# Performance work log

Measured on AMD Instinct MI355X. Metric: run time of the kernel, lower is better.

## Reference

```python
import jax, jax.numpy as jnp
import numpy as np

N_NODES = 100000
N_EDGES = 1600000


def setup_inputs() -> dict:
    key = jax.random.key(0)
    ks = jax.random.split(key, 10)
    return {
        "src": jax.random.randint(ks[0], (N_EDGES,), 0, N_NODES, dtype=jnp.int32),
        "dst": jax.random.randint(ks[1], (N_EDGES,), 0, N_NODES, dtype=jnp.int32),
        "logits": jax.random.normal(ks[2], (N_NODES, 64), jnp.float32),
        "features": jax.random.normal(ks[3], (N_NODES, 512), jnp.float32),
        "proj_W": jax.random.normal(ks[4], (512, 128), jnp.float32) * 0.04,
        "proj_b": jnp.zeros((128,), jnp.float32),
        "deg_table": jax.random.normal(ks[5], (512, 64), jnp.float32) * 0.1,
        "W1": jax.random.normal(ks[6], (256, 128), jnp.float32) * 0.06,
        "b1": jnp.zeros((128,), jnp.float32),
        "W2": jax.random.normal(ks[7], (128, 64), jnp.float32) * 0.09,
        "b2": jnp.zeros((64,), jnp.float32),
    }


def _graph_conv(x, W, b, src, dst, out_deg, in_deg, n):
    # DGL GraphConv, norm='both': scale src by out_deg^-1/2, SpMM sum over
    # edges (src -> dst), scale dst by in_deg^-1/2, then bias. Weight is
    # applied before aggregation when in_feats > out_feats (true here).
    cs = jax.lax.rsqrt(jnp.maximum(out_deg, 1.0))  # [N]
    cd = jax.lax.rsqrt(jnp.maximum(in_deg, 1.0))   # [N]
    h = x * cs[:, None]
    if W.shape[0] > W.shape[1]:
        h = h @ W
        agg = jax.ops.segment_sum(h[src], dst, num_segments=n)
    else:
        agg = jax.ops.segment_sum(h[src], dst, num_segments=n) @ W
    return agg * cd[:, None] + b


def reference(src, dst, logits, features, proj_W, proj_b, deg_table, W1, b1, W2, b2):
    n = logits.shape[0]
    ones = jnp.ones(src.shape, jnp.float32)
    out_deg = jax.ops.segment_sum(ones, src, num_segments=n)  # [N]
    in_deg = jax.ops.segment_sum(ones, dst, num_segments=n)   # [N]

    feat = features @ proj_W + proj_b                          # [N, 128]
    deg_idx = (in_deg + out_deg).astype(jnp.int32)             # [N]
    deg_emb = deg_table[deg_idx]                               # [N, 64]
    x = jnp.concatenate([logits, feat, deg_emb], axis=-1)      # [N, 256]

    x = _graph_conv(x, W1, b1, src, dst, out_deg, in_deg, n)
    x = jax.nn.relu(x)  # dropout omitted (eval mode)
    x = _graph_conv(x, W2, b2, src, dst, out_deg, in_deg, n)
    return x
```

## Files before the change

### kernel.cpp

```cpp
#include <hip/hip_runtime.h>
#include <cstdint>
#include <cstddef>


typedef short short8 __attribute__((ext_vector_type(8)));
typedef float f32x4 __attribute__((ext_vector_type(4)));

__device__ __forceinline__ unsigned short f2bf(float f) {
    unsigned u = __float_as_uint(f);
    u += 0x7fff + ((u >> 16) & 1);
    return (unsigned short)(u >> 16);
}
__device__ __forceinline__ float bf2f(unsigned short s) {
    return __uint_as_float(((unsigned)s) << 16);
}

__device__ __forceinline__ void split_f4(float4 a, float4 b, short8& hv, short8& lv) {
    float f[8] = {a.x, a.y, a.z, a.w, b.x, b.y, b.z, b.w};
#pragma unroll
    for (int i = 0; i < 8; ++i) {
        unsigned u = __float_as_uint(f[i]);
        hv[i] = (short)(u >> 16);
        float r = f[i] - __uint_as_float(u & 0xffff0000u);
        lv[i] = (short)(__float_as_uint(r) >> 16);
    }
}


__global__ __launch_bounds__(256) void k_bcount(
    const int* __restrict__ src, const int* __restrict__ dst, int E,
    int* __restrict__ dcount, int* __restrict__ scount)
{
    __shared__ int dh[128], sh_[128];
    int t = threadIdx.x;
    if (t < 128) { dh[t] = 0; sh_[t] = 0; }
    __syncthreads();
    int e0 = blockIdx.x * 4096;
#pragma unroll
    for (int i = 0; i < 16; ++i) {
        int idx = e0 + t + i * 256;
        if (idx < E) {
            atomicAdd(&dh[dst[idx] >> 10], 1);
            atomicAdd(&sh_[src[idx] >> 10], 1);
        }
    }
    __syncthreads();
    if (t < 128) {
        if (dh[t]) atomicAdd(&dcount[t], dh[t]);
        if (sh_[t]) atomicAdd(&scount[t], sh_[t]);
    }
}

__global__ __launch_bounds__(128) void k_bscan(
    const int* __restrict__ dcount, const int* __restrict__ scount, int nb,
    int E, int* __restrict__ dboff, int* __restrict__ sboff,
    int* __restrict__ dcur, int* __restrict__ scur,
    int* __restrict__ rowp, int N)
{
    __shared__ int sh[128];
    int t = threadIdx.x;
    int v = (t < nb) ? dcount[t] : 0;
    sh[t] = v;
    __syncthreads();
    for (int off = 1; off < 128; off <<= 1) {
        int x = (t >= off) ? sh[t - off] : 0;
        __syncthreads();
        sh[t] += x;
        __syncthreads();
    }
    if (t < nb) { int e = sh[t] - v; dboff[t] = e; dcur[t] = e; }
    __syncthreads();
    int v2 = (t < nb) ? scount[t] : 0;
    sh[t] = v2;
    __syncthreads();
    for (int off = 1; off < 128; off <<= 1) {
        int x = (t >= off) ? sh[t - off] : 0;
        __syncthreads();
        sh[t] += x;
        __syncthreads();
    }
    if (t < nb) { int e = sh[t] - v2; sboff[t] = e; scur[t] = e; }
    if (t == 0) rowp[N] = E;
}

__global__ __launch_bounds__(256) void k_scatter2(
    const int* __restrict__ src, const int* __restrict__ dst, int E,
    int* __restrict__ dcur, int* __restrict__ scur,
    unsigned* __restrict__ ebuf, unsigned short* __restrict__ sbuf, int nb)
{
    __shared__ int dh[128], dbase[128], sh_[128], sbase[128];
    int t = threadIdx.x;
    int e0 = blockIdx.x * 4096;
    if (t < 128) { dh[t] = 0; sh_[t] = 0; }
    __syncthreads();
    int s_[16], d_[16];
#pragma unroll
    for (int i = 0; i < 16; ++i) {
        int idx = e0 + t + i * 256;
        if (idx < E) {
            s_[i] = src[idx];
            d_[i] = dst[idx];
            atomicAdd(&dh[d_[i] >> 10], 1);
            atomicAdd(&sh_[s_[i] >> 10], 1);
        } else d_[i] = -1;
    }
    __syncthreads();
    if (t < nb) {
        if (dh[t]) dbase[t] = atomicAdd(&dcur[t], dh[t]);
        if (sh_[t]) sbase[t] = atomicAdd(&scur[t], sh_[t]);
    }
    __syncthreads();
    if (t < 128) { dh[t] = 0; sh_[t] = 0; }
    __syncthreads();
#pragma unroll
    for (int i = 0; i < 16; ++i) {
        if (d_[i] >= 0) {
            int b = d_[i] >> 10;
            int p = dbase[b] + atomicAdd(&dh[b], 1);
            ebuf[p] = (unsigned)s_[i] | ((unsigned)(d_[i] & 1023) << 17);
            int bs = s_[i] >> 10;
            int q = sbase[bs] + atomicAdd(&sh_[bs], 1);
            sbuf[q] = (unsigned short)(s_[i] & 1023);
        }
    }
}

__global__ __launch_bounds__(512) void k_bucket_dst(
    const unsigned* __restrict__ ebuf, const int* __restrict__ dboff,
    const int* __restrict__ dcount, int* __restrict__ ind,
    int* __restrict__ rowp, int* __restrict__ csr, int N)
{
    __shared__ int cnt[1024];
    __shared__ int sums[512];
    int b = blockIdx.x;
    int nb0 = b << 10;
    int ncnt = min(1024, N - nb0);
    int t = threadIdx.x;
    cnt[t] = 0; cnt[t + 512] = 0;
    __syncthreads();
    int lo = dboff[b], hi = lo + dcount[b];
    for (int idx = lo + t; idx < hi; idx += 512)
        atomicAdd(&cnt[ebuf[idx] >> 17], 1);
    __syncthreads();
    int c0 = cnt[2 * t], c1 = cnt[2 * t + 1];
    sums[t] = c0 + c1;
    __syncthreads();
    for (int off = 1; off < 512; off <<= 1) {
        int x = (t >= off) ? sums[t - off] : 0;
        __syncthreads();
        sums[t] += x;
        __syncthreads();
    }
    int excl = sums[t] - (c0 + c1);
    int r0 = lo + excl, r1 = r0 + c0;
    if (2 * t < ncnt)     { rowp[nb0 + 2 * t] = r0;     ind[nb0 + 2 * t] = c0; }
    if (2 * t + 1 < ncnt) { rowp[nb0 + 2 * t + 1] = r1; ind[nb0 + 2 * t + 1] = c1; }
    __syncthreads();
    cnt[2 * t] = r0; cnt[2 * t + 1] = r1;
    __syncthreads();
    for (int idx = lo + t; idx < hi; idx += 512) {
        unsigned e = ebuf[idx];
        int p = atomicAdd(&cnt[e >> 17], 1);
        csr[p] = (int)(e & 0x1FFFF);
    }
}

__global__ __launch_bounds__(512) void k_bucket_src(
    const unsigned short* __restrict__ sbuf, const int* __restrict__ sboff,
    const int* __restrict__ scount, const int* __restrict__ ind,
    float* __restrict__ cs, float* __restrict__ cd, int* __restrict__ didx,
    int N)
{
    __shared__ int cnt[1024];
    int b = blockIdx.x;
    int nb0 = b << 10;
    int ncnt = min(1024, N - nb0);
    int t = threadIdx.x;
    cnt[t] = 0; cnt[t + 512] = 0;
    __syncthreads();
    int lo = sboff[b], hi = lo + scount[b];
    for (int idx = lo + t; idx < hi; idx += 512)
        atomicAdd(&cnt[sbuf[idx]], 1);
    __syncthreads();
#pragma unroll
    for (int k = 0; k < 2; ++k) {
        int loc = t + k * 512;
        if (loc < ncnt) {
            int od = cnt[loc];
            int id = ind[nb0 + loc];
            cs[nb0 + loc] = rsqrtf((float)(od > 0 ? od : 1));
            cd[nb0 + loc] = rsqrtf((float)(id > 0 ? id : 1));
            int d = od + id;
            didx[nb0 + loc] = d > 511 ? 511 : d;
        }
    }
}

__global__ __launch_bounds__(256) void k_wf(
    const float* __restrict__ projW, const float* __restrict__ projb,
    const float* __restrict__ W1, float* __restrict__ WF,
    float* __restrict__ cb)
{
    if (blockIdx.x == 256) {
        int j = threadIdx.x;
        if (j < 128) {
            float s = 0.f;
            for (int m = 0; m < 128; ++m)
                s = fmaf(projb[m], W1[(size_t)(64 + m) * 128 + j], s);
            cb[j] = s;
        }
        return;
    }
    int idx = blockIdx.x * 256 + threadIdx.x;
    int k = idx >> 7, j = idx & 127;
    const float* a = projW + (size_t)k * 128;
    float s = 0.f;
#pragma unroll 8
    for (int m = 0; m < 128; ++m) s = fmaf(a[m], W1[(size_t)(64 + m) * 128 + j], s);
    WF[idx] = s;
}

__global__ __launch_bounds__(256) void k_wt(
    const float* __restrict__ WF, const float* __restrict__ W1,
    const float* __restrict__ W2,
    unsigned short* __restrict__ wtf_hi, unsigned short* __restrict__ wtf_lo,
    unsigned short* __restrict__ w2tf_hi, unsigned short* __restrict__ w2tf_lo)
{
    int idx = blockIdx.x * 256 + threadIdx.x;
    if (idx < 81920) {
        int e = idx & 7;
        int lane = (idx >> 3) & 63;
        int ci = (idx >> 9) & 7;
        int t = idx >> 12;
        int j = ci * 16 + (lane & 15);
        int k = t * 32 + (lane >> 4) * 8 + e;
        float v;
        if (k < 512) v = WF[(size_t)k * 128 + j];
        else if (k < 576) v = W1[(size_t)(k - 512) * 128 + j];
        else v = W1[(size_t)(192 + (k - 576)) * 128 + j];
        unsigned short h = f2bf(v);
        wtf_hi[idx] = h;
        float r = v - bf2f(h);
        wtf_lo[idx] = (unsigned short)(__float_as_uint(r) >> 16);
    } else if (idx < 90112) {
        int i2 = idx - 81920;
        int e = i2 & 7;
        int lane = (i2 >> 3) & 63;
        int ci = (i2 >> 9) & 3;
        int t = i2 >> 11;
        int j = ci * 16 + (lane & 15);
        int k = t * 32 + (lane >> 4) * 8 + e;
        float v = W2[(size_t)k * 64 + j];
        unsigned short h = f2bf(v);
        w2tf_hi[i2] = h;
        float r = v - bf2f(h);
        w2tf_lo[i2] = (unsigned short)(__float_as_uint(r) >> 16);
    }
}

__global__ __launch_bounds__(256, 4) void k_h1(
    const float* __restrict__ logits, const float* __restrict__ features,
    const float* __restrict__ deg_table, const int* __restrict__ didx,
    const unsigned short* __restrict__ wtf_hi, const unsigned short* __restrict__ wtf_lo,
    const float* __restrict__ cb, const float* __restrict__ cs,
    unsigned short* __restrict__ h1, int N)
{
    constexpr int NT = 20;
    __shared__ __align__(16) short Bh[2][4096];
    __shared__ __align__(16) short Bl[2][4096];
    int tid = threadIdx.x;
    int lane = tid & 63, w = tid >> 6;
    int fr = lane & 15, kg = lane >> 4;
    int i0 = blockIdx.x * 64 + w * 16;
    int r0 = i0 + fr;  if (r0 >= N) r0 = N - 1;
    int dd0 = didx[r0];

    f32x4 acc[8];
#pragma unroll
    for (int ci = 0; ci < 8; ++ci) acc[ci] = (f32x4)0.f;

    auto aptr = [&](int t) -> const float* {
        if (t < 16) return features  + (size_t)r0 * 512 + t * 32 + kg * 8;
        if (t < 18) return logits    + (size_t)r0 * 64 + (t - 16) * 32 + kg * 8;
        return deg_table + (size_t)dd0 * 64 + (t - 18) * 32 + kg * 8;
    };

    float4 ac0, ac1, an0, an1;
    uint4 sbh0, sbh1, sbl0, sbl1;

    {
        const unsigned short* g = wtf_hi + tid * 8;
        sbh0 = *(const uint4*)g;
        sbh1 = *(const uint4*)(g + 2048);
        const unsigned short* g2 = wtf_lo + tid * 8;
        sbl0 = *(const uint4*)g2;
        sbl1 = *(const uint4*)(g2 + 2048);
        *(uint4*)&Bh[0][tid * 8] = sbh0;
        *(uint4*)&Bh[0][2048 + tid * 8] = sbh1;
        *(uint4*)&Bl[0][tid * 8] = sbl0;
        *(uint4*)&Bl[0][2048 + tid * 8] = sbl1;
        const float* p = aptr(0);
        ac0 = *(const float4*)p;  ac1 = *(const float4*)(p + 4);
    }
    __syncthreads();

    for (int t = 0; t < NT; ++t) {
        int cbuf = t & 1;
        if (t + 1 < NT) {
            const unsigned short* g = wtf_hi + (size_t)(t + 1) * 4096 + tid * 8;
            sbh0 = *(const uint4*)g;
            sbh1 = *(const uint4*)(g + 2048);
            const unsigned short* g2 = wtf_lo + (size_t)(t + 1) * 4096 + tid * 8;
            sbl0 = *(const uint4*)g2;
            sbl1 = *(const uint4*)(g2 + 2048);
            const float* p = aptr(t + 1);
            an0 = *(const float4*)p;  an1 = *(const float4*)(p + 4);
        }
        short8 ah, al;
        split_f4(ac0, ac1, ah, al);
#pragma unroll
        for (int ci = 0; ci < 8; ++ci) {
            short8 bh = *(const short8*)&Bh[cbuf][ci * 512 + lane * 8];
            short8 bl = *(const short8*)&Bl[cbuf][ci * 512 + lane * 8];
            acc[ci] = __builtin_amdgcn_mfma_f32_16x16x32_bf16(ah, bh, acc[ci], 0, 0, 0);
            acc[ci] = __builtin_amdgcn_mfma_f32_16x16x32_bf16(al, bh, acc[ci], 0, 0, 0);
            acc[ci] = __builtin_amdgcn_mfma_f32_16x16x32_bf16(ah, bl, acc[ci], 0, 0, 0);
        }
        if (t + 1 < NT) {
            *(uint4*)&Bh[cbuf ^ 1][tid * 8] = sbh0;
            *(uint4*)&Bh[cbuf ^ 1][2048 + tid * 8] = sbh1;
            *(uint4*)&Bl[cbuf ^ 1][tid * 8] = sbl0;
            *(uint4*)&Bl[cbuf ^ 1][2048 + tid * 8] = sbl1;
            ac0 = an0;  ac1 = an1;
        }
        __syncthreads();
    }

    float cbv[8];
#pragma unroll
    for (int ci = 0; ci < 8; ++ci) cbv[ci] = cb[ci * 16 + fr];
#pragma unroll
    for (int j = 0; j < 4; ++j) {
        int row = i0 + kg * 4 + j;
        if (row < N) {
            float scv = cs[row];
#pragma unroll
            for (int ci = 0; ci < 8; ++ci) {
                h1[(size_t)row * 128 + ci * 16 + fr] =
                    f2bf(scv * (acc[ci][j] + cbv[ci]));
            }
        }
    }
}

__global__ __launch_bounds__(256) void k_agg1(
    const unsigned short* __restrict__ h1, const int* __restrict__ rowp,
    const int* __restrict__ csr, const float* __restrict__ cd,
    const float* __restrict__ b1, float* __restrict__ y, int N)
{
    int i = blockIdx.x * 8 + (threadIdx.x >> 5);
    if (i >= N) return;
    int lane = threadIdx.x & 31;
    int s0 = rowp[i], s1 = rowp[i + 1];
    float a0 = 0.f, a1 = 0.f, a2 = 0.f, a3 = 0.f;
    int e = s0;
    for (; e + 8 <= s1; e += 8) {
        uint2 v0 = *(const uint2*)(h1 + (size_t)csr[e + 0] * 128 + lane * 4);
        uint2 v1 = *(const uint2*)(h1 + (size_t)csr[e + 1] * 128 + lane * 4);
        uint2 v2 = *(const uint2*)(h1 + (size_t)csr[e + 2] * 128 + lane * 4);
        uint2 v3 = *(const uint2*)(h1 + (size_t)csr[e + 3] * 128 + lane * 4);
        uint2 v4 = *(const uint2*)(h1 + (size_t)csr[e + 4] * 128 + lane * 4);
        uint2 v5 = *(const uint2*)(h1 + (size_t)csr[e + 5] * 128 + lane * 4);
        uint2 v6 = *(const uint2*)(h1 + (size_t)csr[e + 6] * 128 + lane * 4);
        uint2 v7 = *(const uint2*)(h1 + (size_t)csr[e + 7] * 128 + lane * 4);
        a0 += ((__uint_as_float(v0.x << 16) + __uint_as_float(v1.x << 16)) +
               (__uint_as_float(v2.x << 16) + __uint_as_float(v3.x << 16))) +
              ((__uint_as_float(v4.x << 16) + __uint_as_float(v5.x << 16)) +
               (__uint_as_float(v6.x << 16) + __uint_as_float(v7.x << 16)));
        a1 += ((__uint_as_float(v0.x & 0xffff0000u) + __uint_as_float(v1.x & 0xffff0000u)) +
               (__uint_as_float(v2.x & 0xffff0000u) + __uint_as_float(v3.x & 0xffff0000u))) +
              ((__uint_as_float(v4.x & 0xffff0000u) + __uint_as_float(v5.x & 0xffff0000u)) +
               (__uint_as_float(v6.x & 0xffff0000u) + __uint_as_float(v7.x & 0xffff0000u)));
        a2 += ((__uint_as_float(v0.y << 16) + __uint_as_float(v1.y << 16)) +
               (__uint_as_float(v2.y << 16) + __uint_as_float(v3.y << 16))) +
              ((__uint_as_float(v4.y << 16) + __uint_as_float(v5.y << 16)) +
               (__uint_as_float(v6.y << 16) + __uint_as_float(v7.y << 16)));
        a3 += ((__uint_as_float(v0.y & 0xffff0000u) + __uint_as_float(v1.y & 0xffff0000u)) +
               (__uint_as_float(v2.y & 0xffff0000u) + __uint_as_float(v3.y & 0xffff0000u))) +
              ((__uint_as_float(v4.y & 0xffff0000u) + __uint_as_float(v5.y & 0xffff0000u)) +
               (__uint_as_float(v6.y & 0xffff0000u) + __uint_as_float(v7.y & 0xffff0000u)));
    }
    for (; e < s1; ++e) {
        uint2 v = *(const uint2*)(h1 + (size_t)csr[e] * 128 + lane * 4);
        a0 += __uint_as_float(v.x << 16);
        a1 += __uint_as_float(v.x & 0xffff0000u);
        a2 += __uint_as_float(v.y << 16);
        a3 += __uint_as_float(v.y & 0xffff0000u);
    }
    float cdi = cd[i];
    float4 bv = *(const float4*)(b1 + lane * 4);
    float4 o;
    o.x = fmaxf(fmaf(a0, cdi, bv.x), 0.f);
    o.y = fmaxf(fmaf(a1, cdi, bv.y), 0.f);
    o.z = fmaxf(fmaf(a2, cdi, bv.z), 0.f);
    o.w = fmaxf(fmaf(a3, cdi, bv.w), 0.f);
    *(float4*)(y + (size_t)i * 128 + lane * 4) = o;
}

__global__ __launch_bounds__(256, 3) void k_h2(
    const float* __restrict__ y,
    const unsigned short* __restrict__ w2tf_hi, const unsigned short* __restrict__ w2tf_lo,
    const float* __restrict__ cs, unsigned short* __restrict__ h2, int N)
{
    constexpr int NT = 4;
    __shared__ __align__(16) short B2h[8192];
    __shared__ __align__(16) short B2l[8192];
    int tid = threadIdx.x;
    int lane = tid & 63, w = tid >> 6;
    int fr = lane & 15, kg = lane >> 4;
    int i0 = blockIdx.x * 128 + w * 32;
    int r0 = i0 + fr;       if (r0 >= N) r0 = N - 1;
    int r1 = i0 + 16 + fr;  if (r1 >= N) r1 = N - 1;
    const float* a0 = y + (size_t)r0 * 128 + kg * 8;
    const float* a1 = y + (size_t)r1 * 128 + kg * 8;

#pragma unroll
    for (int i = 0; i < 4; ++i) {
        *(uint4*)&B2h[(i * 256 + tid) * 8] = *(const uint4*)(w2tf_hi + (size_t)(i * 256 + tid) * 8);
        *(uint4*)&B2l[(i * 256 + tid) * 8] = *(const uint4*)(w2tf_lo + (size_t)(i * 256 + tid) * 8);
    }
    __syncthreads();

    f32x4 acc[2][4];
#pragma unroll
    for (int ri = 0; ri < 2; ++ri)
#pragma unroll
        for (int ci = 0; ci < 4; ++ci) acc[ri][ci] = (f32x4)0.f;

    float4 ar00 = *(const float4*)(a0);
    float4 ar01 = *(const float4*)(a0 + 4);
    float4 ar10 = *(const float4*)(a1);
    float4 ar11 = *(const float4*)(a1 + 4);

    for (int t = 0; t < NT; ++t) {
        short8 ah0, al0, ah1, al1;
        split_f4(ar00, ar01, ah0, al0);
        split_f4(ar10, ar11, ah1, al1);
        if (t + 1 < NT) {
            ar00 = *(const float4*)(a0 + (t + 1) * 32);
            ar01 = *(const float4*)(a0 + (t + 1) * 32 + 4);
            ar10 = *(const float4*)(a1 + (t + 1) * 32);
            ar11 = *(const float4*)(a1 + (t + 1) * 32 + 4);
        }
#pragma unroll
        for (int ci = 0; ci < 4; ++ci) {
            short8 bh = *(const short8*)&B2h[((t * 4 + ci) * 64 + lane) * 8];
            short8 bl = *(const short8*)&B2l[((t * 4 + ci) * 64 + lane) * 8];
            acc[0][ci] = __builtin_amdgcn_mfma_f32_16x16x32_bf16(ah0, bh, acc[0][ci], 0, 0, 0);
            acc[0][ci] = __builtin_amdgcn_mfma_f32_16x16x32_bf16(al0, bh, acc[0][ci], 0, 0, 0);
            acc[0][ci] = __builtin_amdgcn_mfma_f32_16x16x32_bf16(ah0, bl, acc[0][ci], 0, 0, 0);
            acc[1][ci] = __builtin_amdgcn_mfma_f32_16x16x32_bf16(ah1, bh, acc[1][ci], 0, 0, 0);
            acc[1][ci] = __builtin_amdgcn_mfma_f32_16x16x32_bf16(al1, bh, acc[1][ci], 0, 0, 0);
            acc[1][ci] = __builtin_amdgcn_mfma_f32_16x16x32_bf16(ah1, bl, acc[1][ci], 0, 0, 0);
        }
    }

#pragma unroll
    for (int ri = 0; ri < 2; ++ri) {
#pragma unroll
        for (int j = 0; j < 4; ++j) {
            int row = i0 + ri * 16 + kg * 4 + j;
            if (row < N) {
                float scv = cs[row];
#pragma unroll
                for (int ci = 0; ci < 4; ++ci) {
                    h2[(size_t)row * 64 + ci * 16 + fr] = f2bf(scv * acc[ri][ci][j]);
                }
            }
        }
    }
}

__global__ __launch_bounds__(256) void k_agg2(
    const unsigned short* __restrict__ h2, const int* __restrict__ rowp,
    const int* __restrict__ csr, const float* __restrict__ cd,
    const float* __restrict__ b2, float* __restrict__ out, int N)
{
    int i = blockIdx.x * 8 + (threadIdx.x >> 5);
    if (i >= N) return;
    int lane = threadIdx.x & 31;
    int s0 = rowp[i], s1 = rowp[i + 1];
    float ax = 0.f, ay = 0.f;
    int e = s0;
    for (; e + 8 <= s1; e += 8) {
        unsigned u0 = *(const unsigned*)(h2 + (size_t)csr[e + 0] * 64 + lane * 2);
        unsigned u1 = *(const unsigned*)(h2 + (size_t)csr[e + 1] * 64 + lane * 2);
        unsigned u2 = *(const unsigned*)(h2 + (size_t)csr[e + 2] * 64 + lane * 2);
        unsigned u3 = *(const unsigned*)(h2 + (size_t)csr[e + 3] * 64 + lane * 2);
        unsigned u4 = *(const unsigned*)(h2 + (size_t)csr[e + 4] * 64 + lane * 2);
        unsigned u5 = *(const unsigned*)(h2 + (size_t)csr[e + 5] * 64 + lane * 2);
        unsigned u6 = *(const unsigned*)(h2 + (size_t)csr[e + 6] * 64 + lane * 2);
        unsigned u7 = *(const unsigned*)(h2 + (size_t)csr[e + 7] * 64 + lane * 2);
        ax += ((__uint_as_float(u0 << 16) + __uint_as_float(u1 << 16)) +
               (__uint_as_float(u2 << 16) + __uint_as_float(u3 << 16))) +
              ((__uint_as_float(u4 << 16) + __uint_as_float(u5 << 16)) +
               (__uint_as_float(u6 << 16) + __uint_as_float(u7 << 16)));
        ay += ((__uint_as_float(u0 & 0xffff0000u) + __uint_as_float(u1 & 0xffff0000u)) +
               (__uint_as_float(u2 & 0xffff0000u) + __uint_as_float(u3 & 0xffff0000u))) +
              ((__uint_as_float(u4 & 0xffff0000u) + __uint_as_float(u5 & 0xffff0000u)) +
               (__uint_as_float(u6 & 0xffff0000u) + __uint_as_float(u7 & 0xffff0000u)));
    }
    for (; e < s1; ++e) {
        unsigned u = *(const unsigned*)(h2 + (size_t)csr[e] * 64 + lane * 2);
        ax += __uint_as_float(u << 16);
        ay += __uint_as_float(u & 0xffff0000u);
    }
    float cdi = cd[i];
    float2 o;
    o.x = fmaf(ax, cdi, b2[lane * 2 + 0]);
    o.y = fmaf(ay, cdi, b2[lane * 2 + 1]);
    *(float2*)(out + (size_t)i * 64 + lane * 2) = o;
}

extern "C" void kernel_launch(void* const* d_in, const int* in_sizes, int n_in,
                              void* d_out, int out_size, void* d_ws, size_t ws_size,
                              hipStream_t stream)
{
    const int* src = (const int*)d_in[0];
    const int* dst = (const int*)d_in[1];
    const float* logits = (const float*)d_in[2];
    const float* features = (const float*)d_in[3];
    const float* projW = (const float*)d_in[4];
    const float* projb = (const float*)d_in[5];
    const float* deg_table = (const float*)d_in[6];
    const float* W1 = (const float*)d_in[7];
    const float* b1 = (const float*)d_in[8];
    const float* W2 = (const float*)d_in[9];
    const float* b2 = (const float*)d_in[10];
    const int E = in_sizes[0];
    const int N = in_sizes[2] / 64;

    char* base = (char*)d_ws;
    size_t off = 0;
    auto alloc = [&](size_t bytes) -> void* {
        void* p = base + off;
        off += (bytes + 255) & ~(size_t)255;
        return p;
    };
    int* ind    = (int*)alloc((size_t)N * 4);
    int* rowp   = (int*)alloc((size_t)(N + 1) * 4);
    int* csr    = (int*)alloc((size_t)E * 4);
    unsigned* ebuf = (unsigned*)alloc((size_t)E * 4);
    unsigned short* sbuf = (unsigned short*)alloc((size_t)E * 2);
    int* didx   = (int*)alloc((size_t)N * 4);
    float* cs   = (float*)alloc((size_t)N * 4);
    float* cd   = (float*)alloc((size_t)N * 4);
    float* WF   = (float*)alloc((size_t)512 * 128 * 4);
    float* cb   = (float*)alloc((size_t)128 * 4);
    int* dcount = (int*)alloc(128 * 4);
    int* scount = (int*)alloc(128 * 4);
    int* dboff  = (int*)alloc(128 * 4);
    int* sboff  = (int*)alloc(128 * 4);
    int* dcur   = (int*)alloc(128 * 4);
    int* scur   = (int*)alloc(128 * 4);
    unsigned short* wtf_hi  = (unsigned short*)alloc((size_t)81920 * 2);
    unsigned short* wtf_lo  = (unsigned short*)alloc((size_t)81920 * 2);
    unsigned short* w2tf_hi = (unsigned short*)alloc((size_t)8192 * 2);
    unsigned short* w2tf_lo = (unsigned short*)alloc((size_t)8192 * 2);
    unsigned short* h1 = (unsigned short*)alloc((size_t)N * 128 * 2);
    float* yb   = (float*)alloc((size_t)N * 128 * 4);
    unsigned short* h2 = h1;
    float* outp = (float*)d_out;

    hipMemsetAsync(dcount, 0, 128 * 4, stream);
    hipMemsetAsync(scount, 0, 128 * 4, stream);

    int mb1 = (N + 63) / 64;
    int mb2 = (N + 127) / 128;
    int ebk = (E + 4095) / 4096;
    int nbuck = (N + 1023) / 1024;

    k_bcount<<<ebk, 256, 0, stream>>>(src, dst, E, dcount, scount);
    k_bscan<<<1, 128, 0, stream>>>(dcount, scount, nbuck, E, dboff, sboff, dcur, scur, rowp, N);
    k_scatter2<<<ebk, 256, 0, stream>>>(src, dst, E, dcur, scur, ebuf, sbuf, nbuck);
    k_bucket_dst<<<nbuck, 512, 0, stream>>>(ebuf, dboff, dcount, ind, rowp, csr, N);
    k_bucket_src<<<nbuck, 512, 0, stream>>>(sbuf, sboff, scount, ind, cs, cd, didx, N);
    k_wf<<<257, 256, 0, stream>>>(projW, projb, W1, WF, cb);
    k_wt<<<352, 256, 0, stream>>>(WF, W1, W2, wtf_hi, wtf_lo, w2tf_hi, w2tf_lo);
    k_h1<<<mb1, 256, 0, stream>>>(logits, features, deg_table, didx, wtf_hi, wtf_lo, cb, cs, h1, N);
    k_agg1<<<(N + 7) / 8, 256, 0, stream>>>(h1, rowp, csr, cd, b1, yb, N);
    k_h2<<<mb2, 256, 0, stream>>>(yb, w2tf_hi, w2tf_lo, cs, h2, N);
    k_agg2<<<(N + 7) / 8, 256, 0, stream>>>(h2, rowp, csr, cd, b2, outp, N);
}
```

Measured before the change: 309.4 us.

## Stage feature tile in swizzled LDS and stream weights directly into registers

The first GEMM kernel now bulk-loads the whole 32x512 feature tile for the block into an XOR-swizzled shared-memory buffer with coalesced float4 loads. It no longer stages weight tiles through double-buffered LDS with per-step barriers. Each wave instead reads its B fragments straight from global memory into a register double buffer, and the logits and degree-embedding fragments are preloaded into registers. Blocks shrink to 128 threads and 32 rows, with launch bounds allowing a single block per CU. This removes per-step syncs and strided feature loads, but uses 64KB of LDS, raises register pressure and lowers occupancy, and makes weight reads redundant across waves.

```diff
diff --git a/kernel.cpp b/kernel.cpp
--- a/kernel.cpp
+++ b/kernel.cpp
@@ -258,82 +258,93 @@
     }
 }
 
-__global__ __launch_bounds__(256, 4) void k_h1(
+__global__ __launch_bounds__(128, 1) void k_h1(
     const float* __restrict__ logits, const float* __restrict__ features,
     const float* __restrict__ deg_table, const int* __restrict__ didx,
     const unsigned short* __restrict__ wtf_hi, const unsigned short* __restrict__ wtf_lo,
     const float* __restrict__ cb, const float* __restrict__ cs,
     unsigned short* __restrict__ h1, int N)
 {
-    constexpr int NT = 20;
-    __shared__ __align__(16) short Bh[2][4096];
-    __shared__ __align__(16) short Bl[2][4096];
+    __shared__ __align__(16) float4 Asm4[4096];
     int tid = threadIdx.x;
     int lane = tid & 63, w = tid >> 6;
     int fr = lane & 15, kg = lane >> 4;
-    int i0 = blockIdx.x * 64 + w * 16;
-    int r0 = i0 + fr;  if (r0 >= N) r0 = N - 1;
+    int i0 = blockIdx.x * 32;
+    int rrel = w * 16 + fr;
+    int r0 = i0 + rrel; if (r0 >= N) r0 = N - 1;
     int dd0 = didx[r0];
 
+    {
+        const float4* gf = (const float4*)features;
+        size_t gmax = (size_t)N * 128 - 1;
+        for (int o = 0; o < 4; ++o) {
+            float4 v[8];
+#pragma unroll
+            for (int c = 0; c < 8; ++c) {
+                size_t gi = (size_t)i0 * 128 + tid + (o * 8 + c) * 128;
+                if (gi > gmax) gi = gmax;
+                v[c] = gf[gi];
+            }
+#pragma unroll
+            for (int c = 0; c < 8; ++c) {
+                int idx = tid + (o * 8 + c) * 128;
+                int row = idx >> 7, cc = idx & 127;
+                Asm4[row * 128 + (cc ^ (row & 7))] = v[c];
+            }
+        }
+    }
+
+    const float* lgp = logits + (size_t)r0 * 64 + kg * 8;
+    const float* dgp = deg_table + (size_t)dd0 * 64 + kg * 8;
+    float4 T0a = *(const float4*)(lgp);
+    float4 T0b = *(const float4*)(lgp + 4);
+    float4 T1a = *(const float4*)(lgp + 32);
+    float4 T1b = *(const float4*)(lgp + 36);
+    float4 T2a = *(const float4*)(dgp);
+    float4 T2b = *(const float4*)(dgp + 4);
+    float4 T3a = *(const float4*)(dgp + 32);
+    float4 T3b = *(const float4*)(dgp + 36);
+
     f32x4 acc[8];
 #pragma unroll
     for (int ci = 0; ci < 8; ++ci) acc[ci] = (f32x4)0.f;
 
-    auto aptr = [&](int t) -> const float* {
-        if (t < 16) return features  + (size_t)r0 * 512 + t * 32 + kg * 8;
-        if (t < 18) return logits    + (size_t)r0 * 64 + (t - 16) * 32 + kg * 8;
-        return deg_table + (size_t)dd0 * 64 + (t - 18) * 32 + kg * 8;
-    };
-
-    float4 ac0, ac1, an0, an1;
-    uint4 sbh0, sbh1, sbl0, sbl1;
-
-    {
-        const unsigned short* g = wtf_hi + tid * 8;
-        sbh0 = *(const uint4*)g;
-        sbh1 = *(const uint4*)(g + 2048);
-        const unsigned short* g2 = wtf_lo + tid * 8;
-        sbl0 = *(const uint4*)g2;
-        sbl1 = *(const uint4*)(g2 + 2048);
-        *(uint4*)&Bh[0][tid * 8] = sbh0;
-        *(uint4*)&Bh[0][2048 + tid * 8] = sbh1;
-        *(uint4*)&Bl[0][tid * 8] = sbl0;
-        *(uint4*)&Bl[0][2048 + tid * 8] = sbl1;
-        const float* p = aptr(0);
-        ac0 = *(const float4*)p;  ac1 = *(const float4*)(p + 4);
-    }
-    __syncthreads();
-
-    for (int t = 0; t < NT; ++t) {
-        int cbuf = t & 1;
-        if (t + 1 < NT) {
-            const unsigned short* g = wtf_hi + (size_t)(t + 1) * 4096 + tid * 8;
-            sbh0 = *(const uint4*)g;
-            sbh1 = *(const uint4*)(g + 2048);
-            const unsigned short* g2 = wtf_lo + (size_t)(t + 1) * 4096 + tid * 8;
-            sbl0 = *(const uint4*)g2;
-            sbl1 = *(const uint4*)(g2 + 2048);
-            const float* p = aptr(t + 1);
-            an0 = *(const float4*)p;  an1 = *(const float4*)(p + 4);
+    uint4 bh[2][8], bl[2][8];
+#pragma unroll
+    for (int ci = 0; ci < 8; ++ci) {
+        bh[0][ci] = *(const uint4*)(wtf_hi + ((size_t)(0 * 8 + ci) * 64 + lane) * 8);
+        bl[0][ci] = *(const uint4*)(wtf_lo + ((size_t)(0 * 8 + ci) * 64 + lane) * 8);
+    }
+    __syncthreads();
+
+#pragma unroll
+    for (int t = 0; t < 20; ++t) {
+        const int s = t & 1;
+        if (t + 1 < 20) {
+#pragma unroll
+            for (int ci = 0; ci < 8; ++ci) {
+                bh[s ^ 1][ci] = *(const uint4*)(wtf_hi + ((size_t)((t + 1) * 8 + ci) * 64 + lane) * 8);
+                bl[s ^ 1][ci] = *(const uint4*)(wtf_lo + ((size_t)((t + 1) * 8 + ci) * 64 + lane) * 8);
+            }
         }
         short8 ah, al;
-        split_f4(ac0, ac1, ah, al);
+        if (t < 16) {
+            int c0 = t * 8 + kg * 2;
+            float4 f0 = Asm4[rrel * 128 + ((c0    ) ^ (rrel & 7))];
+            float4 f1 = Asm4[rrel * 128 + ((c0 + 1) ^ (rrel & 7))];
+            split_f4(f0, f1, ah, al);
+        } else if (t == 16) split_f4(T0a, T0b, ah, al);
+        else if (t == 17) split_f4(T1a, T1b, ah, al);
+        else if (t == 18) split_f4(T2a, T2b, ah, al);
+        else              split_f4(T3a, T3b, ah, al);
 #pragma unroll
         for (int ci = 0; ci < 8; ++ci) {
-            short8 bh = *(const short8*)&Bh[cbuf][ci * 512 + lane * 8];
-            short8 bl = *(const short8*)&Bl[cbuf][ci * 512 + lane * 8];
-            acc[ci] = __builtin_amdgcn_mfma_f32_16x16x32_bf16(ah, bh, acc[ci], 0, 0, 0);
-            acc[ci] = __builtin_amdgcn_mfma_f32_16x16x32_bf16(al, bh, acc[ci], 0, 0, 0);
-            acc[ci] = __builtin_amdgcn_mfma_f32_16x16x32_bf16(ah, bl, acc[ci], 0, 0, 0);
-        }
-        if (t + 1 < NT) {
-            *(uint4*)&Bh[cbuf ^ 1][tid * 8] = sbh0;
-            *(uint4*)&Bh[cbuf ^ 1][2048 + tid * 8] = sbh1;
-            *(uint4*)&Bl[cbuf ^ 1][tid * 8] = sbl0;
-            *(uint4*)&Bl[cbuf ^ 1][2048 + tid * 8] = sbl1;
-            ac0 = an0;  ac1 = an1;
-        }
-        __syncthreads();
+            short8 bhv = *(short8*)&bh[s][ci];
+            short8 blv = *(short8*)&bl[s][ci];
+            acc[ci] = __builtin_amdgcn_mfma_f32_16x16x32_bf16(ah, bhv, acc[ci], 0, 0, 0);
+            acc[ci] = __builtin_amdgcn_mfma_f32_16x16x32_bf16(al, bhv, acc[ci], 0, 0, 0);
+            acc[ci] = __builtin_amdgcn_mfma_f32_16x16x32_bf16(ah, blv, acc[ci], 0, 0, 0);
+        }
     }
 
     float cbv[8];
@@ -341,7 +352,7 @@
     for (int ci = 0; ci < 8; ++ci) cbv[ci] = cb[ci * 16 + fr];
 #pragma unroll
     for (int j = 0; j < 4; ++j) {
-        int row = i0 + kg * 4 + j;
+        int row = i0 + w * 16 + kg * 4 + j;
         if (row < N) {
             float scv = cs[row];
 #pragma unroll
@@ -575,7 +586,7 @@
     hipMemsetAsync(dcount, 0, 128 * 4, stream);
     hipMemsetAsync(scount, 0, 128 * 4, stream);
 
-    int mb1 = (N + 63) / 64;
+    int mb1 = (N + 31) / 32;
     int mb2 = (N + 127) / 128;
     int ebk = (E + 4095) / 4096;
     int nbuck = (N + 1023) / 1024;
@@ -587,7 +598,7 @@
     k_bucket_src<<<nbuck, 512, 0, stream>>>(sbuf, sboff, scount, ind, cs, cd, didx, N);
     k_wf<<<257, 256, 0, stream>>>(projW, projb, W1, WF, cb);
     k_wt<<<352, 256, 0, stream>>>(WF, W1, W2, wtf_hi, wtf_lo, w2tf_hi, w2tf_lo);
-    k_h1<<<mb1, 256, 0, stream>>>(logits, features, deg_table, didx, wtf_hi, wtf_lo, cb, cs, h1, N);
+    k_h1<<<mb1, 128, 0, stream>>>(logits, features, deg_table, didx, wtf_hi, wtf_lo, cb, cs, h1, N);
     k_agg1<<<(N + 7) / 8, 256, 0, stream>>>(h1, rowp, csr, cd, b1, yb, N);
     k_h2<<<mb2, 256, 0, stream>>>(yb, w2tf_hi, w2tf_lo, cs, h2, N);
     k_agg2<<<(N + 7) / 8, 256, 0, stream>>>(h2, rowp, csr, cd, b2, outp, N);
```

New measurement: 479.1 us. 1.55x slower.
